# Performance work log

Measured on AMD Instinct MI355X. Metric: run time of the kernel, lower is better.

The kernel has to match this reference:

```python
import jax, jax.numpy as jnp
import numpy as np

B, C, O, H, W = 8, 256, 256, 64, 64
K = 3  # kernel size


def setup_inputs() -> dict:
    key = jax.random.key(0)
    k1, k2, k3 = jax.random.split(key, 3)
    x = jax.random.normal(k1, (B, C, H, W), dtype=jnp.float32)
    # offset-predicting conv: 18 = 2*K*K output channels (dy,dx per kernel tap).
    # Zero-init in the module; use small random weights so offsets are nontrivial.
    w_off = jax.random.normal(k2, (2 * K * K, C, K, K), dtype=jnp.float32) * 0.01
    b_off = jnp.zeros((2 * K * K,), dtype=jnp.float32)
    # deform conv weight, xavier-uniform (mmcv DeformConv has no bias)
    bound = float(np.sqrt(6.0 / (C * K * K + O * K * K)))
    w_def = jax.random.uniform(k3, (O, C, K, K), dtype=jnp.float32, minval=-bound, maxval=bound)
    return {"x": x, "w_off": w_off, "b_off": b_off, "w_def": w_def}


def _bilinear_gather(x, py, px):
    # x: [B,C,H,W]; py,px: [B,K2,Ho,Wo] float sample coords (zero padding outside)
    # returns [B,C,K2*Ho*Wo]
    Bb, Cc, Hh, Ww = x.shape
    y0f = jnp.floor(py); x0f = jnp.floor(px)
    wy = (py - y0f).reshape(Bb, 1, -1)
    wx = (px - x0f).reshape(Bb, 1, -1)
    y0 = y0f.astype(jnp.int32); x0 = x0f.astype(jnp.int32)
    flat = x.reshape(Bb, Cc, Hh * Ww)

    def gather(yi, xi):
        valid = ((yi >= 0) & (yi < Hh) & (xi >= 0) & (xi < Ww))
        yc = jnp.clip(yi, 0, Hh - 1); xc = jnp.clip(xi, 0, Ww - 1)
        idx = (yc * Ww + xc).reshape(Bb, 1, -1)
        g = jnp.take_along_axis(flat, jnp.broadcast_to(idx, (Bb, Cc, idx.shape[-1])), axis=2)
        return g * valid.reshape(Bb, 1, -1).astype(x.dtype)

    v00 = gather(y0, x0)
    v01 = gather(y0, x0 + 1)
    v10 = gather(y0 + 1, x0)
    v11 = gather(y0 + 1, x0 + 1)
    return (v00 * (1 - wy) * (1 - wx) + v01 * (1 - wy) * wx
            + v10 * wy * (1 - wx) + v11 * wy * wx)


def reference(x, w_off, b_off, w_def):
    # act -> offset conv -> deformable conv (norm = Identity)
    x = jax.nn.relu(x)
    offset = jax.lax.conv_general_dilated(
        x, w_off, (1, 1), ((1, 1), (1, 1)),
        dimension_numbers=('NCHW', 'OIHW', 'NCHW')) + b_off[None, :, None, None]
    Bb, Cc, Hh, Ww = x.shape
    Ho, Wo = offset.shape[2], offset.shape[3]
    K2 = K * K
    # mmcv offset layout: [B, 2*K2, H, W] with (dy, dx) pairs per kernel tap (row-major taps)
    off = offset.reshape(Bb, K2, 2, Ho, Wo)
    ky, kx = jnp.meshgrid(jnp.arange(K), jnp.arange(K), indexing='ij')
    ky = ky.reshape(-1).astype(x.dtype); kx = kx.reshape(-1).astype(x.dtype)
    # base sample positions: out_pos*stride - pad + tap  (stride=1, pad=1)
    base_y = jnp.arange(Ho, dtype=x.dtype)[None, :, None] - 1.0 + ky[:, None, None]  # [K2,Ho,1]
    base_x = jnp.arange(Wo, dtype=x.dtype)[None, None, :] - 1.0 + kx[:, None, None]  # [K2,1,Wo]
    py = base_y + off[:, :, 0]  # [B,K2,Ho,Wo]
    px = base_x + off[:, :, 1]
    samp = _bilinear_gather(x, py, px).reshape(Bb, Cc, K2, Ho, Wo)
    out = jnp.einsum('bckhw,ock->bohw', samp, w_def.reshape(w_def.shape[0], Cc, K2))
    return out
```

## Files before the change

### kernel.cpp

```cpp
#include <hip/hip_runtime.h>
#include <stdint.h>

#define B_ 8
#define C_ 256
#define O_ 256
#define HW_ 4096

typedef __attribute__((ext_vector_type(8))) short bf16x8;
typedef __attribute__((ext_vector_type(4))) float f32x4;

__device__ __forceinline__ unsigned short f2bf(float f) {
    union { float f; unsigned u; } v; v.f = f;
    unsigned r = v.u + 0x7FFFu + ((v.u >> 16) & 1u);
    return (unsigned short)(r >> 16);
}
__device__ __forceinline__ float bf2f(short s) {
    union { unsigned u; float f; } v; v.u = ((unsigned)(unsigned short)s) << 16;
    return v.f;
}

__global__ __launch_bounds__(256) void k_nhwc(const float* __restrict__ x,
                                              unsigned short* __restrict__ xT) {
    int bh = blockIdx.x;
    int b = bh & 7, h = bh >> 3;
    int t = threadIdx.x, px = t & 63, wg = t >> 6;
#pragma unroll
    for (int i = 0; i < 4; ++i) {
        int c0 = i * 64 + wg * 16;
        unsigned short v[16];
#pragma unroll
        for (int j = 0; j < 16; ++j) {
            float f = x[((size_t)(b * C_ + c0 + j)) * HW_ + h * 64 + px];
            v[j] = f2bf(fmaxf(f, 0.f));
        }
        unsigned short* dst = xT + ((size_t)((b * 64 + h) * 64 + px)) * C_ + c0;
        *reinterpret_cast<bf16x8*>(dst) = *reinterpret_cast<const bf16x8*>(v);
        *reinterpret_cast<bf16x8*>(dst + 8) = *reinterpret_cast<const bf16x8*>(v + 8);
    }
}

__global__ void k_prep_wdef(const float* __restrict__ w_def, unsigned short* __restrict__ wfrag) {
    int idx = blockIdx.x * 256 + threadIdx.x;
    if (idx >= 9 * 8 * 16 * 64) return;
    int lane = idx & 63;
    int mfg = (idx >> 6) & 15;
    int ccc = (idx >> 10) & 7;
    int k2 = idx >> 13;
    int o = mfg * 16 + (lane & 15);
    int cb = ccc * 32 + (lane >> 4) * 8;
    bf16x8 pk;
#pragma unroll
    for (int j = 0; j < 8; ++j)
        pk[j] = (short)f2bf(w_def[(size_t)(o * C_ + cb + j) * 9 + k2]);
    *reinterpret_cast<bf16x8*>(wfrag + (size_t)idx * 8) = pk;
}

__global__ void k_prep_woffrag(const float* __restrict__ w_off, unsigned short* __restrict__ wfr) {
    int idx = blockIdx.x * 256 + threadIdx.x;
    if (idx >= 9 * 8 * 2 * 64) return;
    int lane = idx & 63;
    int mfg = (idx >> 6) & 1;
    int ccc = (idx >> 7) & 7;
    int k2 = idx >> 10;
    int o = mfg * 16 + (lane & 15);
    int cb = ccc * 32 + (lane >> 4) * 8;
    bf16x8 pk;
#pragma unroll
    for (int j = 0; j < 8; ++j)
        pk[j] = (o < 18) ? (short)f2bf(w_off[(size_t)(o * C_ + cb + j) * 9 + k2]) : (short)0;
    *reinterpret_cast<bf16x8*>(wfr + (size_t)idx * 8) = pk;
}

__global__ __launch_bounds__(256) void k_offconv3(const unsigned short* __restrict__ xT,
                                                  const unsigned short* __restrict__ wofr,
                                                  const float* __restrict__ b_off,
                                                  float* __restrict__ offs) {
    int bh = blockIdx.x;
    int b = bh & 7, h = bh >> 3;
    int tid = threadIdx.x, lane = tid & 63, wm = tid >> 6;
    int px = wm * 16 + (lane & 15);
    int chl = (lane >> 4) * 8;
    f32x4 acc0 = (f32x4){0.f, 0.f, 0.f, 0.f};
    f32x4 acc1 = (f32x4){0.f, 0.f, 0.f, 0.f};
    const unsigned short* xb = xT + (size_t)b * HW_ * C_;
    const bf16x8 bz = (bf16x8){0, 0, 0, 0, 0, 0, 0, 0};
    for (int k2 = 0; k2 < 9; ++k2) {
        int y = h + k2 / 3 - 1;
        int xs = px + k2 % 3 - 1;
        bool v = ((unsigned)y < 64u) && ((unsigned)xs < 64u);
        int yc = y < 0 ? 0 : (y > 63 ? 63 : y);
        int xc = xs < 0 ? 0 : (xs > 63 ? 63 : xs);
        const unsigned short* xp = xb + (size_t)(yc * 64 + xc) * C_ + chl;
#pragma unroll
        for (int q = 0; q < 8; ++q) {
            bf16x8 bf = *reinterpret_cast<const bf16x8*>(xp + q * 32);
            if (!v) bf = bz;
            const bf16x8* wp = reinterpret_cast<const bf16x8*>(wofr) +
                               (size_t)((k2 * 8 + q) * 2) * 64 + lane;
            acc0 = __builtin_amdgcn_mfma_f32_16x16x32_bf16(wp[0], bf, acc0, 0, 0, 0);
            acc1 = __builtin_amdgcn_mfma_f32_16x16x32_bf16(wp[64], bf, acc1, 0, 0, 0);
        }
    }
#pragma unroll
    for (int r = 0; r < 4; ++r) {
        int oc = (lane >> 4) * 4 + r;
        offs[(((size_t)b * 18 + oc) * 64 + h) * 64 + px] = acc0[r] + b_off[oc];
    }
#pragma unroll
    for (int r = 0; r < 4; ++r) {
        int oc = 16 + (lane >> 4) * 4 + r;
        if (oc < 18)
            offs[(((size_t)b * 18 + oc) * 64 + h) * 64 + px] = acc1[r] + b_off[oc];
    }
}

__global__ __launch_bounds__(256, 2) void k_deform3(const unsigned short* __restrict__ xT,
                                                    const unsigned short* __restrict__ wfrag,
                                                    const float* __restrict__ offs,
                                                    float* __restrict__ out) {
    int bh = blockIdx.x;
    int b = bh & 7, h = bh >> 3;
    int tid = threadIdx.x, lane = tid & 63, wm = tid >> 6;

    __shared__ float s_py[9][64], s_px[9][64];
    __shared__ __align__(16) unsigned short s_samp[2][64 * 64];

    for (int idx = tid; idx < 576; idx += 256) {
        int k2 = idx >> 6, p = idx & 63;
        float dy = offs[(((size_t)b * 18 + k2 * 2 + 0) * 64 + h) * 64 + p];
        float dx = offs[(((size_t)b * 18 + k2 * 2 + 1) * 64 + h) * 64 + p];
        s_py[k2][p] = (float)(h - 1 + k2 / 3) + dy;
        s_px[k2][p] = (float)(p - 1 + k2 % 3) + dx;
    }
    __syncthreads();

    f32x4 acc[4][4];
#pragma unroll
    for (int i = 0; i < 4; ++i)
#pragma unroll
        for (int j = 0; j < 4; ++j) acc[i][j] = (f32x4){0.f, 0.f, 0.f, 0.f};

    const unsigned short* xb = xT + (size_t)b * HW_ * C_;

    float w00, w01, w10, w11;
    int i00, i01, i10, i11;
    bf16x8 a0, a1, a2, a3, a4, a5, a6, a7;

#define GEOM(K2)                                                                  \
    {                                                                             \
        float py = s_py[K2][lane], pxx = s_px[K2][lane];                          \
        float y0f = floorf(py), x0f = floorf(pxx);                                \
        float wy = py - y0f, wx = pxx - x0f;                                      \
        int y0 = (int)y0f, x0 = (int)x0f;                                         \
        w00 = (1.f - wy) * (1.f - wx); w01 = (1.f - wy) * wx;                     \
        w10 = wy * (1.f - wx); w11 = wy * wx;                                     \
        bool vy0 = (unsigned)y0 < 64u, vy1 = (unsigned)(y0 + 1) < 64u;            \
        bool vx0 = (unsigned)x0 < 64u, vx1 = (unsigned)(x0 + 1) < 64u;            \
        if (!(vy0 && vx0)) w00 = 0.f;                                             \
        if (!(vy0 && vx1)) w01 = 0.f;                                             \
        if (!(vy1 && vx0)) w10 = 0.f;                                             \
        if (!(vy1 && vx1)) w11 = 0.f;                                             \
        int y0c = y0 < 0 ? 0 : (y0 > 63 ? 63 : y0);                               \
        int y1c = (y0 + 1) < 0 ? 0 : ((y0 + 1) > 63 ? 63 : (y0 + 1));             \
        int x0c = x0 < 0 ? 0 : (x0 > 63 ? 63 : x0);                               \
        int x1c = (x0 + 1) < 0 ? 0 : ((x0 + 1) > 63 ? 63 : (x0 + 1));             \
        i00 = (y0c * 64 + x0c) * C_; i01 = (y0c * 64 + x1c) * C_;                 \
        i10 = (y1c * 64 + x0c) * C_; i11 = (y1c * 64 + x1c) * C_;                 \
    }

#define ISSUE(S)                                                                  \
    {                                                                             \
        int ch0 = ((S) & 3) * 64 + wm * 8;                                        \
        a0 = *reinterpret_cast<const bf16x8*>(xb + i00 + ch0);                    \
        a1 = *reinterpret_cast<const bf16x8*>(xb + i01 + ch0);                    \
        a2 = *reinterpret_cast<const bf16x8*>(xb + i10 + ch0);                    \
        a3 = *reinterpret_cast<const bf16x8*>(xb + i11 + ch0);                    \
        a4 = *reinterpret_cast<const bf16x8*>(xb + i00 + ch0 + 32);               \
        a5 = *reinterpret_cast<const bf16x8*>(xb + i01 + ch0 + 32);               \
        a6 = *reinterpret_cast<const bf16x8*>(xb + i10 + ch0 + 32);               \
        a7 = *reinterpret_cast<const bf16x8*>(xb + i11 + ch0 + 32);               \
    }

#define PACK(BUF)                                                                 \
    {                                                                             \
        bf16x8 pk0, pk1;                                                          \
        _Pragma("unroll") for (int j = 0; j < 8; ++j)                             \
        {                                                                         \
            float s0 = w00 * bf2f(a0[j]) + w01 * bf2f(a1[j]) +                    \
                       w10 * bf2f(a2[j]) + w11 * bf2f(a3[j]);                     \
            float s1 = w00 * bf2f(a4[j]) + w01 * bf2f(a5[j]) +                    \
                       w10 * bf2f(a6[j]) + w11 * bf2f(a7[j]);                     \
            pk0[j] = (short)f2bf(s0);                                             \
            pk1[j] = (short)f2bf(s1);                                             \
        }                                                                         \
        int sl0 = (wm ^ (lane & 7)) & 7;                                          \
        int sl1 = ((wm + 4) ^ (lane & 7)) & 7;                                    \
        *reinterpret_cast<bf16x8*>(&s_samp[BUF][lane * 64 + sl0 * 8]) = pk0;      \
        *reinterpret_cast<bf16x8*>(&s_samp[BUF][lane * 64 + sl1 * 8]) = pk1;      \
    }

    GEOM(0);
    ISSUE(0);
    PACK(0);

#pragma unroll 2
    for (int s = 0; s < 36; ++s) {
        bf16x8 afr[2][4];
        const bf16x8* wf = reinterpret_cast<const bf16x8*>(wfrag) +
                           (size_t)(s * 2 * 16 + wm * 4) * 64 + lane;
#pragma unroll
        for (int kk = 0; kk < 2; ++kk)
#pragma unroll
            for (int mf = 0; mf < 4; ++mf)
                afr[kk][mf] = wf[(size_t)(kk * 16 + mf) * 64];

        int nxt = s + 1;
        if (nxt < 36) {
            if ((nxt & 3) == 0) GEOM(nxt >> 2);
            ISSUE(nxt);
        }
        __syncthreads();

        bf16x8 bfr[2][4];
        int bsel = s & 1;
#pragma unroll
        for (int kk = 0; kk < 2; ++kk)
#pragma unroll
            for (int nf = 0; nf < 4; ++nf) {
                int n = nf * 16 + (lane & 15);
                int oct = kk * 4 + (lane >> 4);
                int slot = (oct ^ (n & 7)) & 7;
                bfr[kk][nf] = *reinterpret_cast<const bf16x8*>(&s_samp[bsel][n * 64 + slot * 8]);
            }
#pragma unroll
        for (int kk = 0; kk < 2; ++kk)
#pragma unroll
            for (int mf = 0; mf < 4; ++mf)
#pragma unroll
                for (int nf = 0; nf < 4; ++nf)
                    acc[mf][nf] = __builtin_amdgcn_mfma_f32_16x16x32_bf16(
                        afr[kk][mf], bfr[kk][nf], acc[mf][nf], 0, 0, 0);

        if (nxt < 36) PACK(nxt & 1);
    }

    float* op = out + (size_t)b * O_ * HW_ + h * 64;
#pragma unroll
    for (int mf = 0; mf < 4; ++mf)
#pragma unroll
        for (int nf = 0; nf < 4; ++nf)
#pragma unroll
            for (int r = 0; r < 4; ++r) {
                int o = wm * 64 + mf * 16 + (lane >> 4) * 4 + r;
                int w = nf * 16 + (lane & 15);
                op[(size_t)o * HW_ + w] = acc[mf][nf][r];
            }
}

extern "C" void kernel_launch(void* const* d_in, const int* in_sizes, int n_in,
                              void* d_out, int out_size, void* d_ws, size_t ws_size,
                              hipStream_t stream) {
    const float* x = (const float*)d_in[0];
    const float* w_off = (const float*)d_in[1];
    const float* b_off = (const float*)d_in[2];
    const float* w_def = (const float*)d_in[3];
    float* out = (float*)d_out;
    char* ws = (char*)d_ws;

    float* offs = (float*)ws;
    unsigned short* xT = (unsigned short*)(ws + 2359296);
    unsigned short* wfrag = (unsigned short*)(ws + 2359296 + 16777216);
    unsigned short* wofr = (unsigned short*)(ws + 2359296 + 16777216 + 1179648);

    k_nhwc<<<512, 256, 0, stream>>>(x, xT);
    k_prep_wdef<<<288, 256, 0, stream>>>(w_def, wfrag);
    k_prep_woffrag<<<36, 256, 0, stream>>>(w_off, wofr);
    k_offconv3<<<512, 256, 0, stream>>>(xT, wofr, b_off, offs);
    k_deform3<<<512, 256, 0, stream>>>(xT, wfrag, offs, out);
}
```

Measured before the change: 130.6 us.

## Switch to fp16 with packed bilinear math and software-pipeline weight fragment loads

Changes the intermediate NHWC activations, the weight fragments and the MFMA ops from bf16 to fp16. The bilinear blend now runs as packed half-precision vector math instead of scalar bf16→fp32 unpack and repack. The main loop is restructured: PACK moves to the start of each iteration, the next step's weight fragments are prefetched into a second register set, and a raw barrier with an explicit lgkmcnt wait replaces __syncthreads. This targets ALU cost in the gather/pack phase and load latency ahead of the MFMAs, at the cost of fp16 range and precision in the blend and more register pressure.

```diff
diff --git a/kernel.cpp b/kernel.cpp
--- a/kernel.cpp
+++ b/kernel.cpp
@@ -6,40 +6,33 @@
 #define O_ 256
 #define HW_ 4096
 
-typedef __attribute__((ext_vector_type(8))) short bf16x8;
+typedef _Float16 f16x8 __attribute__((ext_vector_type(8)));
+typedef _Float16 f16x2 __attribute__((ext_vector_type(2)));
 typedef __attribute__((ext_vector_type(4))) float f32x4;
 
-__device__ __forceinline__ unsigned short f2bf(float f) {
-    union { float f; unsigned u; } v; v.f = f;
-    unsigned r = v.u + 0x7FFFu + ((v.u >> 16) & 1u);
-    return (unsigned short)(r >> 16);
-}
-__device__ __forceinline__ float bf2f(short s) {
-    union { unsigned u; float f; } v; v.u = ((unsigned)(unsigned short)s) << 16;
-    return v.f;
-}
-
 __global__ __launch_bounds__(256) void k_nhwc(const float* __restrict__ x,
-                                              unsigned short* __restrict__ xT) {
+                                              _Float16* __restrict__ xT) {
     int bh = blockIdx.x;
     int b = bh & 7, h = bh >> 3;
     int t = threadIdx.x, px = t & 63, wg = t >> 6;
 #pragma unroll
     for (int i = 0; i < 4; ++i) {
         int c0 = i * 64 + wg * 16;
-        unsigned short v[16];
-#pragma unroll
-        for (int j = 0; j < 16; ++j) {
-            float f = x[((size_t)(b * C_ + c0 + j)) * HW_ + h * 64 + px];
-            v[j] = f2bf(fmaxf(f, 0.f));
-        }
-        unsigned short* dst = xT + ((size_t)((b * 64 + h) * 64 + px)) * C_ + c0;
-        *reinterpret_cast<bf16x8*>(dst) = *reinterpret_cast<const bf16x8*>(v);
-        *reinterpret_cast<bf16x8*>(dst + 8) = *reinterpret_cast<const bf16x8*>(v + 8);
-    }
-}
-
-__global__ void k_prep_wdef(const float* __restrict__ w_def, unsigned short* __restrict__ wfrag) {
+        f16x8 va, vb;
+#pragma unroll
+        for (int j = 0; j < 8; ++j) {
+            float f0 = x[((size_t)(b * C_ + c0 + j)) * HW_ + h * 64 + px];
+            float f1 = x[((size_t)(b * C_ + c0 + 8 + j)) * HW_ + h * 64 + px];
+            va[j] = (_Float16)fmaxf(f0, 0.f);
+            vb[j] = (_Float16)fmaxf(f1, 0.f);
+        }
+        _Float16* dst = xT + ((size_t)((b * 64 + h) * 64 + px)) * C_ + c0;
+        *reinterpret_cast<f16x8*>(dst) = va;
+        *reinterpret_cast<f16x8*>(dst + 8) = vb;
+    }
+}
+
+__global__ void k_prep_wdef(const float* __restrict__ w_def, _Float16* __restrict__ wfrag) {
     int idx = blockIdx.x * 256 + threadIdx.x;
     if (idx >= 9 * 8 * 16 * 64) return;
     int lane = idx & 63;
@@ -48,14 +41,14 @@
     int k2 = idx >> 13;
     int o = mfg * 16 + (lane & 15);
     int cb = ccc * 32 + (lane >> 4) * 8;
-    bf16x8 pk;
+    f16x8 pk;
 #pragma unroll
     for (int j = 0; j < 8; ++j)
-        pk[j] = (short)f2bf(w_def[(size_t)(o * C_ + cb + j) * 9 + k2]);
-    *reinterpret_cast<bf16x8*>(wfrag + (size_t)idx * 8) = pk;
-}
-
-__global__ void k_prep_woffrag(const float* __restrict__ w_off, unsigned short* __restrict__ wfr) {
+        pk[j] = (_Float16)w_def[(size_t)(o * C_ + cb + j) * 9 + k2];
+    *reinterpret_cast<f16x8*>(wfrag + (size_t)idx * 8) = pk;
+}
+
+__global__ void k_prep_woffrag(const float* __restrict__ w_off, _Float16* __restrict__ wfr) {
     int idx = blockIdx.x * 256 + threadIdx.x;
     if (idx >= 9 * 8 * 2 * 64) return;
     int lane = idx & 63;
@@ -64,15 +57,15 @@
     int k2 = idx >> 10;
     int o = mfg * 16 + (lane & 15);
     int cb = ccc * 32 + (lane >> 4) * 8;
-    bf16x8 pk;
+    f16x8 pk;
 #pragma unroll
     for (int j = 0; j < 8; ++j)
-        pk[j] = (o < 18) ? (short)f2bf(w_off[(size_t)(o * C_ + cb + j) * 9 + k2]) : (short)0;
-    *reinterpret_cast<bf16x8*>(wfr + (size_t)idx * 8) = pk;
-}
-
-__global__ __launch_bounds__(256) void k_offconv3(const unsigned short* __restrict__ xT,
-                                                  const unsigned short* __restrict__ wofr,
+        pk[j] = (o < 18) ? (_Float16)w_off[(size_t)(o * C_ + cb + j) * 9 + k2] : (_Float16)0.f;
+    *reinterpret_cast<f16x8*>(wfr + (size_t)idx * 8) = pk;
+}
+
+__global__ __launch_bounds__(256) void k_offconv4(const _Float16* __restrict__ xT,
+                                                  const _Float16* __restrict__ wofr,
                                                   const float* __restrict__ b_off,
                                                   float* __restrict__ offs) {
     int bh = blockIdx.x;
@@ -82,23 +75,22 @@
     int chl = (lane >> 4) * 8;
     f32x4 acc0 = (f32x4){0.f, 0.f, 0.f, 0.f};
     f32x4 acc1 = (f32x4){0.f, 0.f, 0.f, 0.f};
-    const unsigned short* xb = xT + (size_t)b * HW_ * C_;
-    const bf16x8 bz = (bf16x8){0, 0, 0, 0, 0, 0, 0, 0};
+    const _Float16* xb = xT + (size_t)b * HW_ * C_;
     for (int k2 = 0; k2 < 9; ++k2) {
         int y = h + k2 / 3 - 1;
         int xs = px + k2 % 3 - 1;
         bool v = ((unsigned)y < 64u) && ((unsigned)xs < 64u);
         int yc = y < 0 ? 0 : (y > 63 ? 63 : y);
         int xc = xs < 0 ? 0 : (xs > 63 ? 63 : xs);
-        const unsigned short* xp = xb + (size_t)(yc * 64 + xc) * C_ + chl;
+        const _Float16* xp = xb + (size_t)(yc * 64 + xc) * C_ + chl;
 #pragma unroll
         for (int q = 0; q < 8; ++q) {
-            bf16x8 bf = *reinterpret_cast<const bf16x8*>(xp + q * 32);
-            if (!v) bf = bz;
-            const bf16x8* wp = reinterpret_cast<const bf16x8*>(wofr) +
-                               (size_t)((k2 * 8 + q) * 2) * 64 + lane;
-            acc0 = __builtin_amdgcn_mfma_f32_16x16x32_bf16(wp[0], bf, acc0, 0, 0, 0);
-            acc1 = __builtin_amdgcn_mfma_f32_16x16x32_bf16(wp[64], bf, acc1, 0, 0, 0);
+            f16x8 bf = *reinterpret_cast<const f16x8*>(xp + q * 32);
+            if (!v) bf = (f16x8)(_Float16)0.f;
+            const f16x8* wp = reinterpret_cast<const f16x8*>(wofr) +
+                              (size_t)((k2 * 8 + q) * 2) * 64 + lane;
+            acc0 = __builtin_amdgcn_mfma_f32_16x16x32_f16(wp[0], bf, acc0, 0, 0, 0);
+            acc1 = __builtin_amdgcn_mfma_f32_16x16x32_f16(wp[64], bf, acc1, 0, 0, 0);
         }
     }
 #pragma unroll
@@ -114,8 +106,8 @@
     }
 }
 
-__global__ __launch_bounds__(256, 2) void k_deform3(const unsigned short* __restrict__ xT,
-                                                    const unsigned short* __restrict__ wfrag,
+__global__ __launch_bounds__(256, 2) void k_deform4(const _Float16* __restrict__ xT,
+                                                    const _Float16* __restrict__ wfrag,
                                                     const float* __restrict__ offs,
                                                     float* __restrict__ out) {
     int bh = blockIdx.x;
@@ -123,7 +115,7 @@
     int tid = threadIdx.x, lane = tid & 63, wm = tid >> 6;
 
     __shared__ float s_py[9][64], s_px[9][64];
-    __shared__ __align__(16) unsigned short s_samp[2][64 * 64];
+    __shared__ __align__(16) _Float16 s_samp[2][64 * 64];
 
     for (int idx = tid; idx < 576; idx += 256) {
         int k2 = idx >> 6, p = idx & 63;
@@ -140,11 +132,12 @@
 #pragma unroll
         for (int j = 0; j < 4; ++j) acc[i][j] = (f32x4){0.f, 0.f, 0.f, 0.f};
 
-    const unsigned short* xb = xT + (size_t)b * HW_ * C_;
-
-    float w00, w01, w10, w11;
+    const _Float16* xb = xT + (size_t)b * HW_ * C_;
+
+    _Float16 hw00, hw01, hw10, hw11;
     int i00, i01, i10, i11;
-    bf16x8 a0, a1, a2, a3, a4, a5, a6, a7;
+    f16x8 g0, g1, g2, g3, g4, g5, g6, g7;
+    f16x8 Ac[2][4], An[2][4];
 
 #define GEOM(K2)                                                                  \
     {                                                                             \
@@ -152,14 +145,16 @@
         float y0f = floorf(py), x0f = floorf(pxx);                                \
         float wy = py - y0f, wx = pxx - x0f;                                      \
         int y0 = (int)y0f, x0 = (int)x0f;                                         \
-        w00 = (1.f - wy) * (1.f - wx); w01 = (1.f - wy) * wx;                     \
-        w10 = wy * (1.f - wx); w11 = wy * wx;                                     \
+        float w00 = (1.f - wy) * (1.f - wx), w01 = (1.f - wy) * wx;               \
+        float w10 = wy * (1.f - wx), w11 = wy * wx;                               \
         bool vy0 = (unsigned)y0 < 64u, vy1 = (unsigned)(y0 + 1) < 64u;            \
         bool vx0 = (unsigned)x0 < 64u, vx1 = (unsigned)(x0 + 1) < 64u;            \
         if (!(vy0 && vx0)) w00 = 0.f;                                             \
         if (!(vy0 && vx1)) w01 = 0.f;                                             \
         if (!(vy1 && vx0)) w10 = 0.f;                                             \
         if (!(vy1 && vx1)) w11 = 0.f;                                             \
+        hw00 = (_Float16)w00; hw01 = (_Float16)w01;                               \
+        hw10 = (_Float16)w10; hw11 = (_Float16)w11;                               \
         int y0c = y0 < 0 ? 0 : (y0 > 63 ? 63 : y0);                               \
         int y1c = (y0 + 1) < 0 ? 0 : ((y0 + 1) > 63 ? 63 : (y0 + 1));             \
         int x0c = x0 < 0 ? 0 : (x0 > 63 ? 63 : x0);                               \
@@ -171,58 +166,53 @@
 #define ISSUE(S)                                                                  \
     {                                                                             \
         int ch0 = ((S) & 3) * 64 + wm * 8;                                        \
-        a0 = *reinterpret_cast<const bf16x8*>(xb + i00 + ch0);                    \
-        a1 = *reinterpret_cast<const bf16x8*>(xb + i01 + ch0);                    \
-        a2 = *reinterpret_cast<const bf16x8*>(xb + i10 + ch0);                    \
-        a3 = *reinterpret_cast<const bf16x8*>(xb + i11 + ch0);                    \
-        a4 = *reinterpret_cast<const bf16x8*>(xb + i00 + ch0 + 32);               \
-        a5 = *reinterpret_cast<const bf16x8*>(xb + i01 + ch0 + 32);               \
-        a6 = *reinterpret_cast<const bf16x8*>(xb + i10 + ch0 + 32);               \
-        a7 = *reinterpret_cast<const bf16x8*>(xb + i11 + ch0 + 32);               \
+        g0 = *reinterpret_cast<const f16x8*>(xb + i00 + ch0);                     \
+        g1 = *reinterpret_cast<const f16x8*>(xb + i01 + ch0);                     \
+        g2 = *reinterpret_cast<const f16x8*>(xb + i10 + ch0);                     \
+        g3 = *reinterpret_cast<const f16x8*>(xb + i11 + ch0);                     \
+        g4 = *reinterpret_cast<const f16x8*>(xb + i00 + ch0 + 32);                \
+        g5 = *reinterpret_cast<const f16x8*>(xb + i01 + ch0 + 32);                \
+        g6 = *reinterpret_cast<const f16x8*>(xb + i10 + ch0 + 32);                \
+        g7 = *reinterpret_cast<const f16x8*>(xb + i11 + ch0 + 32);                \
     }
 
 #define PACK(BUF)                                                                 \
     {                                                                             \
-        bf16x8 pk0, pk1;                                                          \
-        _Pragma("unroll") for (int j = 0; j < 8; ++j)                             \
-        {                                                                         \
-            float s0 = w00 * bf2f(a0[j]) + w01 * bf2f(a1[j]) +                    \
-                       w10 * bf2f(a2[j]) + w11 * bf2f(a3[j]);                     \
-            float s1 = w00 * bf2f(a4[j]) + w01 * bf2f(a5[j]) +                    \
-                       w10 * bf2f(a6[j]) + w11 * bf2f(a7[j]);                     \
-            pk0[j] = (short)f2bf(s0);                                             \
-            pk1[j] = (short)f2bf(s1);                                             \
-        }                                                                         \
+        f16x8 pk0 = g0 * hw00 + g1 * hw01 + g2 * hw10 + g3 * hw11;                \
+        f16x8 pk1 = g4 * hw00 + g5 * hw01 + g6 * hw10 + g7 * hw11;                \
         int sl0 = (wm ^ (lane & 7)) & 7;                                          \
         int sl1 = ((wm + 4) ^ (lane & 7)) & 7;                                    \
-        *reinterpret_cast<bf16x8*>(&s_samp[BUF][lane * 64 + sl0 * 8]) = pk0;      \
-        *reinterpret_cast<bf16x8*>(&s_samp[BUF][lane * 64 + sl1 * 8]) = pk1;      \
+        *reinterpret_cast<f16x8*>(&s_samp[BUF][lane * 64 + sl0 * 8]) = pk0;       \
+        *reinterpret_cast<f16x8*>(&s_samp[BUF][lane * 64 + sl1 * 8]) = pk1;       \
+    }
+
+#define LOADA(DST, S)                                                             \
+    {                                                                             \
+        const f16x8* wf = reinterpret_cast<const f16x8*>(wfrag) +                 \
+                          (size_t)((S) * 32 + wm * 4) * 64 + lane;                \
+        _Pragma("unroll") for (int kk = 0; kk < 2; ++kk)                          \
+        _Pragma("unroll") for (int mf = 0; mf < 4; ++mf)                          \
+            DST[kk][mf] = wf[(size_t)(kk * 16 + mf) * 64];                        \
     }
 
     GEOM(0);
     ISSUE(0);
-    PACK(0);
+    LOADA(Ac, 0);
 
 #pragma unroll 2
     for (int s = 0; s < 36; ++s) {
-        bf16x8 afr[2][4];
-        const bf16x8* wf = reinterpret_cast<const bf16x8*>(wfrag) +
-                           (size_t)(s * 2 * 16 + wm * 4) * 64 + lane;
-#pragma unroll
-        for (int kk = 0; kk < 2; ++kk)
-#pragma unroll
-            for (int mf = 0; mf < 4; ++mf)
-                afr[kk][mf] = wf[(size_t)(kk * 16 + mf) * 64];
-
+        PACK(s & 1);
         int nxt = s + 1;
         if (nxt < 36) {
             if ((nxt & 3) == 0) GEOM(nxt >> 2);
             ISSUE(nxt);
-        }
-        __syncthreads();
-
-        bf16x8 bfr[2][4];
-        int bsel = s & 1;
+            LOADA(An, nxt);
+        }
+        asm volatile("s_waitcnt lgkmcnt(0)" ::: "memory");
+        __builtin_amdgcn_s_barrier();
+        __builtin_amdgcn_sched_barrier(0);
+
+        f16x8 bfr[2][4];
 #pragma unroll
         for (int kk = 0; kk < 2; ++kk)
 #pragma unroll
@@ -230,7 +220,7 @@
                 int n = nf * 16 + (lane & 15);
                 int oct = kk * 4 + (lane >> 4);
                 int slot = (oct ^ (n & 7)) & 7;
-                bfr[kk][nf] = *reinterpret_cast<const bf16x8*>(&s_samp[bsel][n * 64 + slot * 8]);
+                bfr[kk][nf] = *reinterpret_cast<const f16x8*>(&s_samp[s & 1][n * 64 + slot * 8]);
             }
 #pragma unroll
         for (int kk = 0; kk < 2; ++kk)
@@ -238,10 +228,16 @@
             for (int mf = 0; mf < 4; ++mf)
 #pragma unroll
                 for (int nf = 0; nf < 4; ++nf)
-                    acc[mf][nf] = __builtin_amdgcn_mfma_f32_16x16x32_bf16(
-                        afr[kk][mf], bfr[kk][nf], acc[mf][nf], 0, 0, 0);
-
-        if (nxt < 36) PACK(nxt & 1);
+                    acc[mf][nf] = __builtin_amdgcn_mfma_f32_16x16x32_f16(
+                        Ac[kk][mf], bfr[kk][nf], acc[mf][nf], 0, 0, 0);
+
+        if (nxt < 36) {
+#pragma unroll
+            for (int kk = 0; kk < 2; ++kk)
+#pragma unroll
+                for (int mf = 0; mf < 4; ++mf)
+                    Ac[kk][mf] = An[kk][mf];
+        }
     }
 
     float* op = out + (size_t)b * O_ * HW_ + h * 64;
@@ -268,13 +264,13 @@
     char* ws = (char*)d_ws;
 
     float* offs = (float*)ws;
-    unsigned short* xT = (unsigned short*)(ws + 2359296);
-    unsigned short* wfrag = (unsigned short*)(ws + 2359296 + 16777216);
-    unsigned short* wofr = (unsigned short*)(ws + 2359296 + 16777216 + 1179648);
+    _Float16* xT = (_Float16*)(ws + 2359296);
+    _Float16* wfrag = (_Float16*)(ws + 2359296 + 16777216);
+    _Float16* wofr = (_Float16*)(ws + 2359296 + 16777216 + 1179648);
 
     k_nhwc<<<512, 256, 0, stream>>>(x, xT);
     k_prep_wdef<<<288, 256, 0, stream>>>(w_def, wfrag);
     k_prep_woffrag<<<36, 256, 0, stream>>>(w_off, wofr);
-    k_offconv3<<<512, 256, 0, stream>>>(xT, wofr, b_off, offs);
-    k_deform3<<<512, 256, 0, stream>>>(xT, wfrag, offs, out);
-}
+    k_offconv4<<<512, 256, 0, stream>>>(xT, wofr, b_off, offs);
+    k_deform4<<<512, 256, 0, stream>>>(xT, wfrag, offs, out);
+}
```

After: 134.8 us. 3.2% more time.
